# Kernel tuning notes

Hardware: AMD Instinct MI355X
Metric: run time of the kernel (lower is better)

## Reference

```python
import jax, jax.numpy as jnp
import numpy as np

NUM_REL = 5
NUM_BASES = 8
HID = 128
OUT = 64
IN_FEAT = 256
N_PER_TYPE = 50000
N_NODES = 2 * N_PER_TYPE
N_EDGES = 1000000
EPS = 1e-5  # PairNorm eps


def setup_inputs() -> dict:
    key = jax.random.key(0)
    ks = jax.random.split(key, 14)
    inp = {
        "x_author": jax.random.normal(ks[0], (N_PER_TYPE, IN_FEAT), jnp.float32),
        "x_paper": jax.random.normal(ks[1], (N_PER_TYPE, IN_FEAT), jnp.float32),
        "edge_index": jax.random.randint(ks[2], (2, N_EDGES), 0, N_NODES, jnp.int32),
        "edge_type": jax.random.randint(ks[3], (N_EDGES,), 0, NUM_REL, jnp.int32),
        # per-node-type input projections (nn.Linear)
        "proj_author_w": jax.random.normal(ks[4], (IN_FEAT, HID), jnp.float32) / np.sqrt(IN_FEAT),
        "proj_author_b": jnp.zeros((HID,), jnp.float32),
        "proj_paper_w": jax.random.normal(ks[5], (IN_FEAT, HID), jnp.float32) / np.sqrt(IN_FEAT),
        "proj_paper_b": jnp.zeros((HID,), jnp.float32),
        # RGCNConv layer 0 (hidden -> hidden), basis decomposition, root weight, no bias
        "comp0": jax.random.normal(ks[6], (NUM_REL, NUM_BASES), jnp.float32) / np.sqrt(NUM_BASES),
        "basis0": jax.random.normal(ks[7], (NUM_BASES, HID, HID), jnp.float32) / np.sqrt(HID),
        "root0": jax.random.normal(ks[8], (HID, HID), jnp.float32) / np.sqrt(HID),
        # RGCNConv layer 1 (hidden -> out)
        "comp1": jax.random.normal(ks[9], (NUM_REL, NUM_BASES), jnp.float32) / np.sqrt(NUM_BASES),
        "basis1": jax.random.normal(ks[10], (NUM_BASES, HID, OUT), jnp.float32) / np.sqrt(HID),
        "root1": jax.random.normal(ks[11], (HID, OUT), jnp.float32) / np.sqrt(HID),
    }
    return inp


def pairnorm(x):
    # PyG PairNorm (scale=1, scale_individually=False)
    x = x - x.mean(axis=0, keepdims=True)
    return x / jnp.sqrt(EPS + (x * x).sum(-1).mean())


def rgcn_conv(x, edge_index, edge_type, comp, basis, root):
    # weight[r] = sum_b comp[r,b] * basis[b]  -> [R, Fin, Fout]
    W = jnp.einsum('rb,bio->rio', comp, basis)
    src, dst = edge_index[0], edge_index[1]
    msgs = x[src]                                   # [E, Fin] gather
    seg = dst * NUM_REL + edge_type                 # per (node, relation) segment
    agg = jax.ops.segment_sum(msgs, seg, num_segments=N_NODES * NUM_REL)
    agg = agg.reshape(N_NODES, NUM_REL, -1)         # [N, R, Fin]
    cnt = jax.ops.segment_sum(jnp.ones((msgs.shape[0],), x.dtype), seg,
                              num_segments=N_NODES * NUM_REL).reshape(N_NODES, NUM_REL)
    mean = agg / jnp.maximum(cnt, 1.0)[..., None]   # mean aggregation (0 if no edges)
    return jnp.einsum('nrf,rfo->no', mean, W) + x @ root


def reference(x_author, x_paper, edge_index, edge_type,
              proj_author_w, proj_author_b, proj_paper_w, proj_paper_b,
              comp0, basis0, root0, comp1, basis1, root1):
    h_a = jax.nn.relu(x_author @ proj_author_w + proj_author_b)
    h_p = jax.nn.relu(x_paper @ proj_paper_w + proj_paper_b)
    x = jnp.concatenate([h_a, h_p], axis=0)         # [N, HID]
    x = jax.nn.relu(rgcn_conv(x, edge_index, edge_type, comp0, basis0, root0))
    x = pairnorm(x)
    x_latent = x
    x = rgcn_conv(x, edge_index, edge_type, comp1, basis1, root1)
    x = pairnorm(x)
    return (x, x_latent)
```

## Files before the change

kernel.cpp:

```cpp
#include <hip/hip_runtime.h>
#include <hip/hip_bf16.h>

constexpr int NPT    = 50000;
constexpr int NN     = 100000;
constexpr int NE     = 1000000;
constexpr int HID    = 128;
constexpr int OUTF   = 64;
constexpr int INF    = 256;
constexpr int NREL   = 5;
constexpr int NSEG   = NN * NREL;

typedef __attribute__((ext_vector_type(8))) short short8v;
typedef __attribute__((ext_vector_type(4))) float f32x4;

__device__ __forceinline__ ushort f2bf(float x) {
    uint u = __builtin_bit_cast(uint, x);
    uint r = (u + 0x7FFFu + ((u >> 16) & 1u)) >> 16;
    return (ushort)r;
}
__device__ __forceinline__ float bfhi(uint raw) {
    return __builtin_bit_cast(float, raw & 0xFFFF0000u);
}
__device__ __forceinline__ float bflo(uint raw) {
    return __builtin_bit_cast(float, raw << 16);
}

__device__ __forceinline__ void build_wbT_body(const float* __restrict__ comp,
                                               const float* __restrict__ basis,
                                               const float* __restrict__ root,
                                               ushort* __restrict__ wbT,
                                               int fout, int passOff, int idx) {
    int col = idx >> 7, k = idx & 127;
    float v;
    if (col < 320) {
        int r = col >> 6, f = (col & 63) + passOff;
        v = 0.f;
#pragma unroll
        for (int b = 0; b < 8; b++)
            v += comp[r * 8 + b] * basis[(b * 128 + k) * fout + f];
    } else {
        v = root[k * fout + (col - 320) + passOff];
    }
    wbT[col * 128 + k] = f2bf(v);
}

__global__ void prep_kernel(const float* __restrict__ comp0, const float* __restrict__ basis0,
                            const float* __restrict__ root0,
                            const float* __restrict__ comp1, const float* __restrict__ basis1,
                            const float* __restrict__ root1,
                            const float* __restrict__ paw, const float* __restrict__ ppw,
                            ushort* __restrict__ wbT0a, ushort* __restrict__ wbT0b,
                            ushort* __restrict__ wbT1,
                            ushort* __restrict__ wpa, ushort* __restrict__ wpp,
                            int* __restrict__ cnt, float* __restrict__ statscr,
                            int* __restrict__ recs_pad) {
    const int b = blockIdx.x, t = threadIdx.x;
    if (b < 1954) {
        int i = b * 256 + t;
        if (i < NSEG) cnt[i] = 0;
    } else if (b < 1979) {
        statscr[(b - 1954) * 256 + t] = 0.f;
    } else if (b == 1979) {
        if (t < 128) recs_pad[t] = 0;
    } else if (b < 2172) {
        build_wbT_body(comp0, basis0, root0, wbT0a, HID, 0, (b - 1980) * 256 + t);
    } else if (b < 2364) {
        build_wbT_body(comp0, basis0, root0, wbT0b, HID, 64, (b - 2172) * 256 + t);
    } else if (b < 2556) {
        build_wbT_body(comp1, basis1, root1, wbT1, OUTF, 0, (b - 2364) * 256 + t);
    } else if (b < 2684) {
        int i = (b - 2556) * 256 + t;
        wpa[(size_t)(i & 127) * 256 + (i >> 7)] = f2bf(paw[i]);
    } else {
        int i = (b - 2684) * 256 + t;
        wpp[(size_t)(i & 127) * 256 + (i >> 7)] = f2bf(ppw[i]);
    }
}

__launch_bounds__(256)
__global__ void proj_hist(const float* __restrict__ xa, const float* __restrict__ xp,
                          const ushort* __restrict__ wTa, const ushort* __restrict__ wTp,
                          const float* __restrict__ ba, const float* __restrict__ bp,
                          ushort* __restrict__ x0b,
                          const int* __restrict__ ei, const int* __restrict__ et,
                          int* __restrict__ cnt, int* __restrict__ rank) {
    __shared__ ushort sx[16][264];
    __shared__ ushort so[16][132];
    const int tid = threadIdx.x;
    if (blockIdx.x >= 1250) {
        int e = (blockIdx.x - 1250) * 256 + tid;
        if (e < NE) {
            int seg = ei[NE + e] * NREL + et[e];
            rank[e] = atomicAdd(&cnt[seg], 1);
        }
        return;
    }
    const bool author = blockIdx.x < 625;
    const int tile0 = (blockIdx.x - (author ? 0 : 625)) * 5;
    const float* x = author ? xa : xp;
    const ushort* wT = author ? wTa : wTp;
    const float* bias = author ? ba : bp;
    const int typeBase = author ? 0 : NPT;

    const int wave = tid >> 6, lane = tid & 63;
    const int row = lane & 15, g = lane >> 4;
    const int fcol = wave * 32 + row;

    const ushort* wp0 = wT + (size_t)fcol * 256 + g * 8;
    short8v bA[8], bB[8];
#pragma unroll
    for (int kk = 0; kk < 8; kk++) bA[kk] = *(const short8v*)&wp0[kk * 32];
#pragma unroll
    for (int kk = 0; kk < 8; kk++) bB[kk] = *(const short8v*)&wp0[16 * 256 + kk * 32];
    const float bv0 = bias[fcol], bv1 = bias[fcol + 16];

    const int sr = tid >> 4, part = tid & 15;
    const int fnode = tid >> 4, fb = (tid & 15) * 8;

    for (int t = 0; t < 5; t++) {
        const int nloc = (tile0 + t) * 16;
        {
            size_t rowoff = (size_t)(nloc + sr) * INF + part * 16;
#pragma unroll
            for (int ii = 0; ii < 4; ii++) {
                float4 v = *(const float4*)&x[rowoff + ii * 4];
                ushort4 h = {f2bf(v.x), f2bf(v.y), f2bf(v.z), f2bf(v.w)};
                *(ushort4*)&sx[sr][part * 16 + ii * 4] = h;
            }
        }
        __syncthreads();
        short8v a[8];
#pragma unroll
        for (int kk = 0; kk < 8; kk++) a[kk] = *(const short8v*)&sx[row][kk * 32 + g * 8];
        {
            f32x4 acc0 = {0.f, 0.f, 0.f, 0.f};
            f32x4 acc1 = {0.f, 0.f, 0.f, 0.f};
#pragma unroll
            for (int kk = 0; kk < 8; kk++) {
                acc0 = __builtin_amdgcn_mfma_f32_16x16x32_bf16(a[kk], bA[kk], acc0, 0, 0, 0);
                acc1 = __builtin_amdgcn_mfma_f32_16x16x32_bf16(a[kk], bB[kk], acc1, 0, 0, 0);
            }
#pragma unroll
            for (int q = 0; q < 4; q++) {
                so[g * 4 + q][fcol]      = f2bf(fmaxf(acc0[q] + bv0, 0.f));
                so[g * 4 + q][fcol + 16] = f2bf(fmaxf(acc1[q] + bv1, 0.f));
            }
        }
        __syncthreads();
        {
            ushort4 v0 = *(const ushort4*)&so[fnode][fb];
            ushort4 v1 = *(const ushort4*)&so[fnode][fb + 4];
            size_t gbase = (size_t)(typeBase + nloc + fnode) * 128 + fb;
            *(ushort4*)&x0b[gbase] = v0;
            *(ushort4*)&x0b[gbase + 4] = v1;
        }
    }
}

__global__ void scan1(const int* __restrict__ cnt, int* __restrict__ offs,
                      int* __restrict__ bsums, int n) {
    __shared__ int lds[256];
    const int t = threadIdx.x;
    const int base = blockIdx.x * 2048 + t * 8;
    int vals[8];
    int s = 0;
#pragma unroll
    for (int v = 0; v < 8; v++) {
        int idx = base + v;
        vals[v] = (idx < n) ? cnt[idx] : 0;
        s += vals[v];
    }
    lds[t] = s;
    __syncthreads();
    for (int off = 1; off < 256; off <<= 1) {
        int x = lds[t];
        int y = (t >= off) ? lds[t - off] : 0;
        __syncthreads();
        lds[t] = x + y;
        __syncthreads();
    }
    int run = (t > 0) ? lds[t - 1] : 0;
    if (t == 255) bsums[blockIdx.x] = lds[255];
#pragma unroll
    for (int v = 0; v < 8; v++) {
        int idx = base + v;
        if (idx < n) offs[idx] = run;
        run += vals[v];
    }
}

__global__ void scan2(const int* __restrict__ bsums, int* __restrict__ bsums2, int nb) {
    __shared__ int lds[256];
    const int t = threadIdx.x;
    lds[t] = (t < nb) ? bsums[t] : 0;
    __syncthreads();
    for (int off = 1; off < 256; off <<= 1) {
        int x = lds[t];
        int y = (t >= off) ? lds[t - off] : 0;
        __syncthreads();
        lds[t] = x + y;
        __syncthreads();
    }
    if (t < nb) bsums2[t] = (t > 0) ? lds[t - 1] : 0;
}

__global__ void scan3_desc(const int* __restrict__ offs, const int* __restrict__ bsums2,
                           const int* __restrict__ cnt, int2* __restrict__ desc, int n) {
    int i = blockIdx.x * blockDim.x + threadIdx.x;
    if (i < n) {
        int2 d = {offs[i] + bsums2[i >> 11], cnt[i]};
        desc[i] = d;
    }
}

__launch_bounds__(256)
__global__ void gemm0_scatter(const ushort* __restrict__ xin,
                              const ushort* __restrict__ wbT_a, const ushort* __restrict__ wbT_b,
                              ushort* __restrict__ ytab, float* __restrict__ hout,
                              const int* __restrict__ ei, const int* __restrict__ et,
                              const int* __restrict__ rank,
                              const int2* __restrict__ desc, int2* __restrict__ recs) {
    __shared__ ushort sx[32][136];
    __shared__ ushort so[32][328];
    __shared__ float sroot[32][68];
    const int tid = threadIdx.x;
    if (blockIdx.x >= 1250) {
        int e = (blockIdx.x - 1250) * 256 + tid;
        if (e < NE) {
            int src = ei[e];
            int dst = ei[NE + e];
            int r = et[e];
            int2 d = desc[dst * NREL + r];
            int c = d.y;
            float sc = 1.f / (float)((c > 1) ? c : 1);
            int2 rec = {r * NN + src, __builtin_bit_cast(int, sc)};
            recs[d.x + rank[e]] = rec;
        }
        return;
    }
    const bool first = blockIdx.x < 625;
    const int tile0 = (first ? blockIdx.x : blockIdx.x - 625) * 5;
    const ushort* wbT = first ? wbT_a : wbT_b;
    const int outOff = first ? 0 : 64;
    const int wave = tid >> 6, lane = tid & 63;
    const int row = lane & 15, g = lane >> 4;
    const int wbase = wave * 96;

    const ushort* wp = wbT + (size_t)(wbase + row) * 128 + g * 8;
    short8v B[6][4];
#pragma unroll
    for (int t = 0; t < 6; t++)
#pragma unroll
        for (int kk = 0; kk < 4; kk++)
            B[t][kk] = *(const short8v*)&wp[t * 2048 + kk * 32];

    const int sr = tid >> 3, scl = (tid & 7) * 16;
    const int fnode = tid >> 3, fb = (tid & 7) * 8;

    for (int tt = 0; tt < 5; tt++) {
        const int n0 = (tile0 + tt) * 32;
        {
            const ushort* src = &xin[(size_t)(n0 + sr) * 128 + scl];
            *(short8v*)&sx[sr][scl] = *(const short8v*)&src[0];
            *(short8v*)&sx[sr][scl + 8] = *(const short8v*)&src[8];
        }
        __syncthreads();

        short8v a[2][4];
#pragma unroll
        for (int m = 0; m < 2; m++)
#pragma unroll
            for (int kk = 0; kk < 4; kk++)
                a[m][kk] = *(const short8v*)&sx[m * 16 + row][kk * 32 + g * 8];

#pragma unroll
        for (int t = 0; t < 6; t++) {
            f32x4 acc0 = {0.f, 0.f, 0.f, 0.f};
            f32x4 acc1 = {0.f, 0.f, 0.f, 0.f};
#pragma unroll
            for (int kk = 0; kk < 4; kk++) {
                acc0 = __builtin_amdgcn_mfma_f32_16x16x32_bf16(a[0][kk], B[t][kk], acc0, 0, 0, 0);
                acc1 = __builtin_amdgcn_mfma_f32_16x16x32_bf16(a[1][kk], B[t][kk], acc1, 0, 0, 0);
            }
            const int col = wbase + t * 16 + row;
            if (col < 320) {
#pragma unroll
                for (int q = 0; q < 4; q++) {
                    so[g * 4 + q][col] = f2bf(acc0[q]);
                    so[16 + g * 4 + q][col] = f2bf(acc1[q]);
                }
            } else {
                const int f = col - 320;
#pragma unroll
                for (int q = 0; q < 4; q++) {
                    sroot[g * 4 + q][f] = acc0[q];
                    sroot[16 + g * 4 + q][f] = acc1[q];
                }
            }
        }
        __syncthreads();

        {
#pragma unroll
            for (int r = 0; r < NREL; r++) {
                short8v v = *(const short8v*)&so[fnode][r * 64 + fb];
                *(short8v*)&ytab[(size_t)r * NN * 128 + (size_t)(n0 + fnode) * 128
                                 + outOff + fb] = v;
            }
            float4 r0 = *(const float4*)&sroot[fnode][fb];
            float4 r1 = *(const float4*)&sroot[fnode][fb + 4];
            float* hp = &hout[(size_t)(n0 + fnode) * HID + outOff + fb];
            *(float4*)&hp[0] = r0;
            *(float4*)&hp[4] = r1;
        }
    }
}

__launch_bounds__(256)
__global__ void ytab_gemm1(float* __restrict__ h0x, const float* __restrict__ mu,
                           const ushort* __restrict__ wbT,
                           ushort* __restrict__ ytab, float* __restrict__ h1) {
    __shared__ ushort sx[32][136];
    __shared__ ushort so[32][328];
    __shared__ float sroot[32][68];
    const int tid = threadIdx.x;
    const int tile0 = blockIdx.x * 5;
    const int wave = tid >> 6, lane = tid & 63;
    const int row = lane & 15, g = lane >> 4;
    const int wbase = wave * 96;

    const ushort* wp = wbT + (size_t)(wbase + row) * 128 + g * 8;
    short8v B[6][4];
#pragma unroll
    for (int t = 0; t < 6; t++)
#pragma unroll
        for (int kk = 0; kk < 4; kk++)
            B[t][kk] = *(const short8v*)&wp[t * 2048 + kk * 32];

    const int sr = tid >> 3, scl = (tid & 7) * 16;
    const int fnode = tid >> 3, fb = (tid & 7) * 8;

    float m[16];
#pragma unroll
    for (int i = 0; i < 16; i++) m[i] = mu[scl + i];
    const float s = mu[128];

    for (int tt = 0; tt < 5; tt++) {
        const int n0 = (tile0 + tt) * 32;
        {
            float* hp = &h0x[(size_t)(n0 + sr) * 128 + scl];
            float v[16];
#pragma unroll
            for (int i = 0; i < 4; i++) {
                float4 t4 = *(const float4*)&hp[i * 4];
                v[i * 4 + 0] = (t4.x - m[i * 4 + 0]) * s;
                v[i * 4 + 1] = (t4.y - m[i * 4 + 1]) * s;
                v[i * 4 + 2] = (t4.z - m[i * 4 + 2]) * s;
                v[i * 4 + 3] = (t4.w - m[i * 4 + 3]) * s;
            }
            ushort hb[16];
#pragma unroll
            for (int i = 0; i < 16; i++) hb[i] = f2bf(v[i]);
#pragma unroll
            for (int i = 0; i < 4; i++) {
                float4 t4 = {v[i * 4], v[i * 4 + 1], v[i * 4 + 2], v[i * 4 + 3]};
                *(float4*)&hp[i * 4] = t4;
            }
            *(short8v*)&sx[sr][scl] = *(const short8v*)&hb[0];
            *(short8v*)&sx[sr][scl + 8] = *(const short8v*)&hb[8];
        }
        __syncthreads();

        short8v a[2][4];
#pragma unroll
        for (int mi = 0; mi < 2; mi++)
#pragma unroll
            for (int kk = 0; kk < 4; kk++)
                a[mi][kk] = *(const short8v*)&sx[mi * 16 + row][kk * 32 + g * 8];

#pragma unroll
        for (int t = 0; t < 6; t++) {
            f32x4 acc0 = {0.f, 0.f, 0.f, 0.f};
            f32x4 acc1 = {0.f, 0.f, 0.f, 0.f};
#pragma unroll
            for (int kk = 0; kk < 4; kk++) {
                acc0 = __builtin_amdgcn_mfma_f32_16x16x32_bf16(a[0][kk], B[t][kk], acc0, 0, 0, 0);
                acc1 = __builtin_amdgcn_mfma_f32_16x16x32_bf16(a[1][kk], B[t][kk], acc1, 0, 0, 0);
            }
            const int col = wbase + t * 16 + row;
            if (col < 320) {
#pragma unroll
                for (int q = 0; q < 4; q++) {
                    so[g * 4 + q][col] = f2bf(acc0[q]);
                    so[16 + g * 4 + q][col] = f2bf(acc1[q]);
                }
            } else {
                const int f = col - 320;
#pragma unroll
                for (int q = 0; q < 4; q++) {
                    sroot[g * 4 + q][f] = acc0[q];
                    sroot[16 + g * 4 + q][f] = acc1[q];
                }
            }
        }
        __syncthreads();

        {
#pragma unroll
            for (int r = 0; r < NREL; r++) {
                short8v v = *(const short8v*)&so[fnode][r * 64 + fb];
                *(short8v*)&ytab[(size_t)r * NN * 64 + (size_t)(n0 + fnode) * 64 + fb] = v;
            }
            float4 r0 = *(const float4*)&sroot[fnode][fb];
            float4 r1 = *(const float4*)&sroot[fnode][fb + 4];
            float* hp = &h1[(size_t)(n0 + fnode) * OUTF + fb];
            *(float4*)&hp[0] = r0;
            *(float4*)&hp[4] = r1;
        }
    }
}

template <int FW, bool RELU>
__launch_bounds__(256)
__global__ void agg_kernel(const ushort* __restrict__ ytab,
                           const int2* __restrict__ recs,
                           const int2* __restrict__ desc,
                           float* __restrict__ hout,
                           float* __restrict__ csrep, float* __restrict__ ssrep) {
    constexpr int FPL = FW / 16;
    __shared__ float sred[4][16][FPL + 1];
    const int tid = threadIdx.x;
    const int wave = tid >> 6, lane = tid & 63;
    const int q = lane >> 4, fl = lane & 15;
    const int n0 = blockIdx.x * 16 + wave * 4;

    int start[4], total[4];
#pragma unroll
    for (int rep = 0; rep < 4; rep++) {
        const int s5 = (n0 + rep) * NREL;
        int2 d0 = desc[s5];
        int2 d4 = desc[s5 + 4];
        start[rep] = d0.x;
        total[rep] = d4.x + d4.y - d0.x;
    }
    float hpre[4][FPL];
#pragma unroll
    for (int rep = 0; rep < 4; rep++) {
        const float* hp = &hout[(size_t)(n0 + rep) * FW + fl * FPL];
#pragma unroll
        for (int k = 0; k < FPL; k++) hpre[rep][k] = hp[k];
    }
    int2 rec[4];
#pragma unroll
    for (int rep = 0; rep < 4; rep++) rec[rep] = recs[start[rep] + lane];

    float cs_loc[FPL];
#pragma unroll
    for (int k = 0; k < FPL; k++) cs_loc[k] = 0.f;
    float ss_loc = 0.f;

#pragma unroll
    for (int rep = 0; rep < 4; rep++) {
        float acc[FPL];
#pragma unroll
        for (int k = 0; k < FPL; k++) acc[k] = 0.f;
        const int lim = (total[rep] > 64) ? 64 : total[rep];
        const int iters = (lim + 3) >> 2;
#pragma unroll 2
        for (int it = 0; it < iters; it++) {
            const int j4 = it * 4 + q;
            int rwr = __shfl(rec[rep].x, j4);
            int scb = __shfl(rec[rep].y, j4);
            const bool ok = j4 < lim;
            const int rw = ok ? rwr : 0;
            const float sc = ok ? __builtin_bit_cast(float, scb) : 0.f;
            if (FW == 128) {
                uint4 raw = *(const uint4*)&ytab[(size_t)rw * FW + fl * 8];
                acc[0] += sc * bflo(raw.x); acc[1] += sc * bfhi(raw.x);
                acc[2] += sc * bflo(raw.y); acc[3] += sc * bfhi(raw.y);
                acc[4] += sc * bflo(raw.z); acc[5] += sc * bfhi(raw.z);
                acc[6] += sc * bflo(raw.w); acc[7] += sc * bfhi(raw.w);
            } else {
                uint2 raw = *(const uint2*)&ytab[(size_t)rw * FW + fl * 4];
                acc[0] += sc * bflo(raw.x); acc[1] += sc * bfhi(raw.x);
                acc[2] += sc * bflo(raw.y); acc[3] += sc * bfhi(raw.y);
            }
        }
        if (total[rep] > 64) {
            for (int j = 64 + q; j < total[rep]; j += 4) {
                int2 r2 = recs[start[rep] + j];
                float sc = __builtin_bit_cast(float, r2.y);
                if (FW == 128) {
                    uint4 raw = *(const uint4*)&ytab[(size_t)r2.x * FW + fl * 8];
                    acc[0] += sc * bflo(raw.x); acc[1] += sc * bfhi(raw.x);
                    acc[2] += sc * bflo(raw.y); acc[3] += sc * bfhi(raw.y);
                    acc[4] += sc * bflo(raw.z); acc[5] += sc * bfhi(raw.z);
                    acc[6] += sc * bflo(raw.w); acc[7] += sc * bfhi(raw.w);
                } else {
                    uint2 raw = *(const uint2*)&ytab[(size_t)r2.x * FW + fl * 4];
                    acc[0] += sc * bflo(raw.x); acc[1] += sc * bfhi(raw.x);
                    acc[2] += sc * bflo(raw.y); acc[3] += sc * bfhi(raw.y);
                }
            }
        }
#pragma unroll
        for (int k = 0; k < FPL; k++) {
            acc[k] += __shfl_xor(acc[k], 32);
            acc[k] += __shfl_xor(acc[k], 16);
        }
        if (q == 0) {
            float o[FPL];
#pragma unroll
            for (int k = 0; k < FPL; k++) {
                o[k] = hpre[rep][k] + acc[k];
                if (RELU) o[k] = fmaxf(o[k], 0.f);
                cs_loc[k] += o[k];
                ss_loc += o[k] * o[k];
            }
            float* hp = &hout[(size_t)(n0 + rep) * FW + fl * FPL];
#pragma unroll
            for (int k = 0; k < FPL; k += 4)
                *(float4*)&hp[k] = *(float4*)&o[k];
        }
    }

    if (q == 0) {
#pragma unroll
        for (int k = 0; k < FPL; k++) sred[wave][fl][k] = cs_loc[k];
        sred[wave][fl][FPL] = ss_loc;
    }
    __syncthreads();
    const int repl = blockIdx.x & 31;
    if (tid < FW) {
        int k = tid & (FPL - 1), f2 = tid / FPL;
        float sv = sred[0][f2][k] + sred[1][f2][k] + sred[2][f2][k] + sred[3][f2][k];
        atomicAdd(&csrep[repl * FW + f2 * FPL + k], sv);
    }
    if (tid < 16) {
        float ssv = sred[0][tid][FPL] + sred[1][tid][FPL]
                  + sred[2][tid][FPL] + sred[3][tid][FPL];
#pragma unroll
        for (int mof = 8; mof > 0; mof >>= 1) ssv += __shfl_xor(ssv, mof);
        if (tid == 0) atomicAdd(&ssrep[repl], ssv);
    }
}

template <int F>
__global__ void finalize_rep(const float* __restrict__ csrep,
                             const float* __restrict__ ssrep,
                             float* __restrict__ mu_inv) {
    __shared__ float sred[128];
    const int f = threadIdx.x;
    float s = 0.f;
    for (int r = 0; r < 32; r++) s += csrep[r * F + f];
    float mu = s / (float)NN;
    mu_inv[f] = mu;
    sred[f] = mu * mu;
    __syncthreads();
    for (int h = F / 2; h > 0; h >>= 1) {
        if (f < h) sred[f] += sred[f + h];
        __syncthreads();
    }
    if (f == 0) {
        float ss = 0.f;
        for (int r = 0; r < 32; r++) ss += ssrep[r];
        float var = ss / (float)NN - sred[0];
        mu_inv[F] = rsqrtf(1e-5f + var);
    }
}

template <int F>
__global__ void normalize_kernel(const float* __restrict__ x,
                                 const float* __restrict__ mu_inv,
                                 float* __restrict__ out, int total4) {
    int i = blockIdx.x * blockDim.x + threadIdx.x;
    if (i < total4) {
        int base = i * 4;
        int f = base & (F - 1);
        float4 v = *(const float4*)&x[base];
        float4 m = *(const float4*)&mu_inv[f];
        float s = mu_inv[F];
        float4 o = {(v.x - m.x) * s, (v.y - m.y) * s, (v.z - m.z) * s, (v.w - m.w) * s};
        *(float4*)&out[base] = o;
    }
}

extern "C" void kernel_launch(void* const* d_in, const int* in_sizes, int n_in,
                              void* d_out, int out_size, void* d_ws, size_t ws_size,
                              hipStream_t stream) {
    const float* xa    = (const float*)d_in[0];
    const float* xp    = (const float*)d_in[1];
    const int*   ei    = (const int*)d_in[2];
    const int*   et    = (const int*)d_in[3];
    const float* paw   = (const float*)d_in[4];
    const float* pab   = (const float*)d_in[5];
    const float* ppw   = (const float*)d_in[6];
    const float* ppb   = (const float*)d_in[7];
    const float* comp0 = (const float*)d_in[8];
    const float* basis0= (const float*)d_in[9];
    const float* root0 = (const float*)d_in[10];
    const float* comp1 = (const float*)d_in[11];
    const float* basis1= (const float*)d_in[12];
    const float* root1 = (const float*)d_in[13];
    float* out = (float*)d_out;

    char* ws = (char*)d_ws;
    size_t o = 0;
    auto alloc = [&](size_t b) { size_t p = o; o += (b + 255) & ~(size_t)255; return p; };
    ushort* x0b    = (ushort*)(ws + alloc((size_t)NN * HID * 2));
    ushort* ytab   = (ushort*)(ws + alloc((size_t)NREL * NN * 128 * 2));
    int2*   desc   = (int2*)(ws + alloc((size_t)NSEG * 8));
    int2*   recs   = (int2*)(ws + alloc((size_t)(NE + 64) * 8));
    int*    rank   = (int*)(ws + alloc((size_t)NE * 4));
    ushort* wbT0a  = (ushort*)(ws + alloc(384 * 128 * 2));
    ushort* wbT0b  = (ushort*)(ws + alloc(384 * 128 * 2));
    ushort* wbT1   = (ushort*)(ws + alloc(384 * 128 * 2));
    ushort* wpa    = (ushort*)(ws + alloc(128 * 256 * 2));
    ushort* wpp    = (ushort*)(ws + alloc(128 * 256 * 2));
    float*  statscr= (float*)(ws + alloc(6400 * 4));
    float*  mu0    = (float*)(ws + alloc(129 * 4));
    float*  mu1    = (float*)(ws + alloc(65 * 4));
    float* cs0rep = statscr;
    float* ss0rep = statscr + 4096;
    float* cs1rep = statscr + 4128;
    float* ss1rep = statscr + 6176;

    char* ybase = (char*)ytab;
    int* cnt    = (int*)(ybase);
    int* offs   = (int*)(ybase + (size_t)NSEG * 4);
    int* bsums  = (int*)(ybase + (size_t)NSEG * 8);
    int* bsums2 = (int*)(ybase + (size_t)NSEG * 8 + 4096);

    float* h0 = out + (size_t)NN * OUTF;
    float* h1 = out;

    prep_kernel<<<2812, 256, 0, stream>>>(comp0, basis0, root0, comp1, basis1, root1,
                                          paw, ppw, wbT0a, wbT0b, wbT1, wpa, wpp,
                                          cnt, statscr, (int*)(recs + NE));
    proj_hist<<<1250 + (NE + 255) / 256, 256, 0, stream>>>(xa, xp, wpa, wpp, pab, ppb,
                                                           x0b, ei, et, cnt, rank);

    const int nb = (NSEG + 2047) / 2048;
    scan1<<<nb, 256, 0, stream>>>(cnt, offs, bsums, NSEG);
    scan2<<<1, 256, 0, stream>>>(bsums, bsums2, nb);
    scan3_desc<<<(NSEG + 255) / 256, 256, 0, stream>>>(offs, bsums2, cnt, desc, NSEG);

    gemm0_scatter<<<1250 + (NE + 255) / 256, 256, 0, stream>>>(
        x0b, wbT0a, wbT0b, ytab, h0, ei, et, rank, desc, recs);
    agg_kernel<128, true><<<NN / 16, 256, 0, stream>>>(ytab, recs, desc, h0, cs0rep, ss0rep);
    finalize_rep<128><<<1, 128, 0, stream>>>(cs0rep, ss0rep, mu0);

    ytab_gemm1<<<625, 256, 0, stream>>>(h0, mu0, wbT1, ytab, h1);
    agg_kernel<64, false><<<NN / 16, 256, 0, stream>>>(ytab, recs, desc, h1, cs1rep, ss1rep);
    finalize_rep<64><<<1, 64, 0, stream>>>(cs1rep, ss1rep, mu1);
    normalize_kernel<OUTF><<<(NN * OUTF / 4 + 255) / 256, 256, 0, stream>>>(h1, mu1, out,
                                                                            NN * OUTF / 4);
}
```

Before: 345.5 us.

## Interleave GEMM and edge blocks in fused kernels; store root-term seeds as bf16

```diff
diff --git a/kernel.cpp b/kernel.cpp
--- a/kernel.cpp
+++ b/kernel.cpp
@@ -9,6 +9,7 @@
 constexpr int INF    = 256;
 constexpr int NREL   = 5;
 constexpr int NSEG   = NN * NREL;
+constexpr int NEB    = (NE + 255) / 256;
 
 typedef __attribute__((ext_vector_type(8))) short short8v;
 typedef __attribute__((ext_vector_type(4))) float f32x4;
@@ -87,16 +88,21 @@
     __shared__ ushort sx[16][264];
     __shared__ ushort so[16][132];
     const int tid = threadIdx.x;
-    if (blockIdx.x >= 1250) {
-        int e = (blockIdx.x - 1250) * 256 + tid;
+    const int gid = blockIdx.x;
+    if ((gid & 3) != 0) {
+        int ord = gid - (gid >> 2) - 1;
+        if (ord >= NEB) return;
+        int e = ord * 256 + tid;
         if (e < NE) {
             int seg = ei[NE + e] * NREL + et[e];
             rank[e] = atomicAdd(&cnt[seg], 1);
         }
         return;
     }
-    const bool author = blockIdx.x < 625;
-    const int tile0 = (blockIdx.x - (author ? 0 : 625)) * 5;
+    const int pord = gid >> 2;
+    if (pord >= 1250) return;
+    const bool author = pord < 625;
+    const int tile0 = (pord - (author ? 0 : 625)) * 5;
     const float* x = author ? xa : xp;
     const ushort* wT = author ? wTa : wTp;
     const float* bias = author ? ba : bp;
@@ -216,7 +222,7 @@
 __launch_bounds__(256)
 __global__ void gemm0_scatter(const ushort* __restrict__ xin,
                               const ushort* __restrict__ wbT_a, const ushort* __restrict__ wbT_b,
-                              ushort* __restrict__ ytab, float* __restrict__ hout,
+                              ushort* __restrict__ ytab, ushort* __restrict__ seed0,
                               const int* __restrict__ ei, const int* __restrict__ et,
                               const int* __restrict__ rank,
                               const int2* __restrict__ desc, int2* __restrict__ recs) {
@@ -224,8 +230,11 @@
     __shared__ ushort so[32][328];
     __shared__ float sroot[32][68];
     const int tid = threadIdx.x;
-    if (blockIdx.x >= 1250) {
-        int e = (blockIdx.x - 1250) * 256 + tid;
+    const int gid = blockIdx.x;
+    if ((gid & 3) != 0) {
+        int ord = gid - (gid >> 2) - 1;
+        if (ord >= NEB) return;
+        int e = ord * 256 + tid;
         if (e < NE) {
             int src = ei[e];
             int dst = ei[NE + e];
@@ -238,8 +247,10 @@
         }
         return;
     }
-    const bool first = blockIdx.x < 625;
-    const int tile0 = (first ? blockIdx.x : blockIdx.x - 625) * 5;
+    const int gord = gid >> 2;
+    if (gord >= 1250) return;
+    const bool first = gord < 625;
+    const int tile0 = (first ? gord : gord - 625) * 5;
     const ushort* wbT = first ? wbT_a : wbT_b;
     const int outOff = first ? 0 : 64;
     const int wave = tid >> 6, lane = tid & 63;
@@ -309,9 +320,10 @@
             }
             float4 r0 = *(const float4*)&sroot[fnode][fb];
             float4 r1 = *(const float4*)&sroot[fnode][fb + 4];
-            float* hp = &hout[(size_t)(n0 + fnode) * HID + outOff + fb];
-            *(float4*)&hp[0] = r0;
-            *(float4*)&hp[4] = r1;
+            ushort sb[8] = {f2bf(r0.x), f2bf(r0.y), f2bf(r0.z), f2bf(r0.w),
+                            f2bf(r1.x), f2bf(r1.y), f2bf(r1.z), f2bf(r1.w)};
+            *(short8v*)&seed0[(size_t)(n0 + fnode) * 128 + outOff + fb] =
+                *(const short8v*)sb;
         }
     }
 }
@@ -319,7 +331,7 @@
 __launch_bounds__(256)
 __global__ void ytab_gemm1(float* __restrict__ h0x, const float* __restrict__ mu,
                            const ushort* __restrict__ wbT,
-                           ushort* __restrict__ ytab, float* __restrict__ h1) {
+                           ushort* __restrict__ ytab, ushort* __restrict__ seed1) {
     __shared__ ushort sx[32][136];
     __shared__ ushort so[32][328];
     __shared__ float sroot[32][68];
@@ -413,9 +425,9 @@
             }
             float4 r0 = *(const float4*)&sroot[fnode][fb];
             float4 r1 = *(const float4*)&sroot[fnode][fb + 4];
-            float* hp = &h1[(size_t)(n0 + fnode) * OUTF + fb];
-            *(float4*)&hp[0] = r0;
-            *(float4*)&hp[4] = r1;
+            ushort sb[8] = {f2bf(r0.x), f2bf(r0.y), f2bf(r0.z), f2bf(r0.w),
+                            f2bf(r1.x), f2bf(r1.y), f2bf(r1.z), f2bf(r1.w)};
+            *(short8v*)&seed1[(size_t)(n0 + fnode) * 64 + fb] = *(const short8v*)sb;
         }
     }
 }
@@ -423,6 +435,7 @@
 template <int FW, bool RELU>
 __launch_bounds__(256)
 __global__ void agg_kernel(const ushort* __restrict__ ytab,
+                           const ushort* __restrict__ seed,
                            const int2* __restrict__ recs,
                            const int2* __restrict__ desc,
                            float* __restrict__ hout,
@@ -446,9 +459,17 @@
     float hpre[4][FPL];
 #pragma unroll
     for (int rep = 0; rep < 4; rep++) {
-        const float* hp = &hout[(size_t)(n0 + rep) * FW + fl * FPL];
-#pragma unroll
-        for (int k = 0; k < FPL; k++) hpre[rep][k] = hp[k];
+        if (FW == 128) {
+            uint4 sraw = *(const uint4*)&seed[(size_t)(n0 + rep) * FW + fl * 8];
+            hpre[rep][0] = bflo(sraw.x); hpre[rep][1] = bfhi(sraw.x);
+            hpre[rep][2] = bflo(sraw.y); hpre[rep][3] = bfhi(sraw.y);
+            hpre[rep][4] = bflo(sraw.z); hpre[rep][5] = bfhi(sraw.z);
+            hpre[rep][6] = bflo(sraw.w); hpre[rep][7] = bfhi(sraw.w);
+        } else {
+            uint2 sraw = *(const uint2*)&seed[(size_t)(n0 + rep) * FW + fl * 4];
+            hpre[rep][0] = bflo(sraw.x); hpre[rep][1] = bfhi(sraw.x);
+            hpre[rep][2] = bflo(sraw.y); hpre[rep][3] = bfhi(sraw.y);
+        }
     }
     int2 rec[4];
 #pragma unroll
@@ -609,6 +630,8 @@
     auto alloc = [&](size_t b) { size_t p = o; o += (b + 255) & ~(size_t)255; return p; };
     ushort* x0b    = (ushort*)(ws + alloc((size_t)NN * HID * 2));
     ushort* ytab   = (ushort*)(ws + alloc((size_t)NREL * NN * 128 * 2));
+    ushort* seed0  = (ushort*)(ws + alloc((size_t)NN * HID * 2));
+    ushort* seed1  = (ushort*)(ws + alloc((size_t)NN * OUTF * 2));
     int2*   desc   = (int2*)(ws + alloc((size_t)NSEG * 8));
     int2*   recs   = (int2*)(ws + alloc((size_t)(NE + 64) * 8));
     int*    rank   = (int*)(ws + alloc((size_t)NE * 4));
@@ -637,21 +660,23 @@
     prep_kernel<<<2812, 256, 0, stream>>>(comp0, basis0, root0, comp1, basis1, root1,
                                           paw, ppw, wbT0a, wbT0b, wbT1, wpa, wpp,
                                           cnt, statscr, (int*)(recs + NE));
-    proj_hist<<<1250 + (NE + 255) / 256, 256, 0, stream>>>(xa, xp, wpa, wpp, pab, ppb,
-                                                           x0b, ei, et, cnt, rank);
+    proj_hist<<<5210, 256, 0, stream>>>(xa, xp, wpa, wpp, pab, ppb,
+                                        x0b, ei, et, cnt, rank);
 
     const int nb = (NSEG + 2047) / 2048;
     scan1<<<nb, 256, 0, stream>>>(cnt, offs, bsums, NSEG);
     scan2<<<1, 256, 0, stream>>>(bsums, bsums2, nb);
     scan3_desc<<<(NSEG + 255) / 256, 256, 0, stream>>>(offs, bsums2, cnt, desc, NSEG);
 
-    gemm0_scatter<<<1250 + (NE + 255) / 256, 256, 0, stream>>>(
-        x0b, wbT0a, wbT0b, ytab, h0, ei, et, rank, desc, recs);
-    agg_kernel<128, true><<<NN / 16, 256, 0, stream>>>(ytab, recs, desc, h0, cs0rep, ss0rep);
+    gemm0_scatter<<<5210, 256, 0, stream>>>(x0b, wbT0a, wbT0b, ytab, seed0,
+                                            ei, et, rank, desc, recs);
+    agg_kernel<128, true><<<NN / 16, 256, 0, stream>>>(ytab, seed0, recs, desc, h0,
+                                                       cs0rep, ss0rep);
     finalize_rep<128><<<1, 128, 0, stream>>>(cs0rep, ss0rep, mu0);
 
-    ytab_gemm1<<<625, 256, 0, stream>>>(h0, mu0, wbT1, ytab, h1);
-    agg_kernel<64, false><<<NN / 16, 256, 0, stream>>>(ytab, recs, desc, h1, cs1rep, ss1rep);
+    ytab_gemm1<<<625, 256, 0, stream>>>(h0, mu0, wbT1, ytab, seed1);
+    agg_kernel<64, false><<<NN / 16, 256, 0, stream>>>(ytab, seed1, recs, desc, h1,
+                                                       cs1rep, ss1rep);
     finalize_rep<64><<<1, 64, 0, stream>>>(cs1rep, ss1rep, mu1);
     normalize_kernel<OUTF><<<(NN * OUTF / 4 + 255) / 256, 256, 0, stream>>>(h1, mu1, out,
                                                                             NN * OUTF / 4);
```

After: 452.9 us. 1.31x slower.
